# Optimization experiments

Measured on AMD Instinct MI355X. Metric: run time of the kernel, lower is better.

The kernel has to match this reference:

```python
import jax, jax.numpy as jnp
import numpy as np

B, T, D, H = 4, 2048, 1024, 16
HD = D // H  # head_size = 64
EPS = 1e-5


def layernorm(x, g, b):
    mu = jnp.mean(x, axis=-1, keepdims=True)
    var = jnp.var(x, axis=-1, keepdims=True)
    return (x - mu) * jax.lax.rsqrt(var + EPS) * g + b


def setup_inputs() -> dict:
    key = jax.random.key(0)
    ks = jax.random.split(key, 8)
    s = 0.02
    return {
        "x": jax.random.normal(ks[0], (B, T, D), jnp.float32),
        "Wq": jax.random.normal(ks[1], (D, D), jnp.float32) * s,
        "Wk": jax.random.normal(ks[2], (D, D), jnp.float32) * s,
        "Wv": jax.random.normal(ks[3], (D, D), jnp.float32) * s,
        "Wo": jax.random.normal(ks[4], (D, D), jnp.float32) * s,
        "bo": jnp.zeros((D,), jnp.float32),
        "W1": jax.random.normal(ks[5], (D, 4 * D), jnp.float32) * s,
        "b1": jnp.zeros((4 * D,), jnp.float32),
        "W2": jax.random.normal(ks[6], (4 * D, D), jnp.float32) * s,
        "b2": jnp.zeros((D,), jnp.float32),
        "ln1_g": jnp.ones((D,), jnp.float32),
        "ln1_b": jnp.zeros((D,), jnp.float32),
        "ln2_g": jnp.ones((D,), jnp.float32),
        "ln2_b": jnp.zeros((D,), jnp.float32),
    }


def reference(x, Wq, Wk, Wv, Wo, bo, W1, b1, W2, b2, ln1_g, ln1_b, ln2_g, ln2_b):
    # --- multi-head causal self-attention (pre-LN), dropout off (eval) ---
    h = layernorm(x, ln1_g, ln1_b)
    q = jnp.einsum('btd,de->bte', h, Wq).reshape(B, T, H, HD)
    k = jnp.einsum('btd,de->bte', h, Wk).reshape(B, T, H, HD)
    v = jnp.einsum('btd,de->bte', h, Wv).reshape(B, T, H, HD)
    scores = jnp.einsum('bqhd,bkhd->bhqk', q, k) * (HD ** -0.5)
    causal = jnp.tril(jnp.ones((T, T), bool))
    scores = jnp.where(causal, scores, -jnp.inf)
    attn = jax.nn.softmax(scores, axis=-1)
    out = jnp.einsum('bhqk,bkhd->bqhd', attn, v).reshape(B, T, D)
    out = jnp.einsum('btd,de->bte', out, Wo) + bo
    x = x + out
    # --- feed-forward: Linear -> ReLU -> Linear -> ReLU (as in source) ---
    h2 = layernorm(x, ln2_g, ln2_b)
    ff = jax.nn.relu(jnp.einsum('btd,df->btf', h2, W1) + b1)
    ff = jax.nn.relu(jnp.einsum('btf,fd->btd', ff, W2) + b2)
    return x + ff
```

## Files before the change

### kernel.cpp

```cpp
#include <hip/hip_runtime.h>
#include <cstdint>
#include <cstddef>

typedef unsigned short u16;
typedef __attribute__((ext_vector_type(8))) short bf16x8;
typedef __attribute__((ext_vector_type(4))) float f32x4;
typedef __attribute__((address_space(1))) const unsigned int gu32;
typedef __attribute__((address_space(3))) unsigned int lu32;

#define QSCALE 0.1803368801111204f

__device__ __forceinline__ u16 f2bf(float f) {
  uint32_t u = __float_as_uint(f);
  u += 0x7fffu + ((u >> 16) & 1u);
  return (u16)(u >> 16);
}

__global__ __launch_bounds__(256) void transpose_w(const float* __restrict__ W,
                                                   u16* __restrict__ WT,
                                                   int K, int N) {
  __shared__ float t[32][33];
  int n0 = blockIdx.x * 32, k0 = blockIdx.y * 32;
  for (int i = threadIdx.y; i < 32; i += 8)
    t[i][threadIdx.x] = W[(size_t)(k0 + i) * N + n0 + threadIdx.x];
  __syncthreads();
  for (int i = threadIdx.y; i < 32; i += 8)
    WT[(size_t)(n0 + i) * K + k0 + threadIdx.x] = f2bf(t[threadIdx.x][i]);
}

__global__ __launch_bounds__(256) void ln_kernel(const float* __restrict__ x,
                                                 const float* __restrict__ g,
                                                 const float* __restrict__ b,
                                                 u16* __restrict__ out) {
  int row = blockIdx.x;
  const float4 v = *(const float4*)(x + (size_t)row * 1024 + threadIdx.x * 4);
  float s = v.x + v.y + v.z + v.w;
  float ss = v.x * v.x + v.y * v.y + v.z * v.z + v.w * v.w;
#pragma unroll
  for (int d = 1; d < 64; d <<= 1) { s += __shfl_xor(s, d); ss += __shfl_xor(ss, d); }
  __shared__ float rs_[4], rss_[4];
  int wv = threadIdx.x >> 6;
  if ((threadIdx.x & 63) == 0) { rs_[wv] = s; rss_[wv] = ss; }
  __syncthreads();
  s = rs_[0] + rs_[1] + rs_[2] + rs_[3];
  ss = rss_[0] + rss_[1] + rss_[2] + rss_[3];
  float mu = s * (1.f / 1024.f);
  float var = ss * (1.f / 1024.f) - mu * mu;
  float rstd = rsqrtf(var + 1e-5f);
  float4 gv = *(const float4*)(g + threadIdx.x * 4);
  float4 bv = *(const float4*)(b + threadIdx.x * 4);
  uint32_t lo = (uint32_t)f2bf((v.x - mu) * rstd * gv.x + bv.x) |
                ((uint32_t)f2bf((v.y - mu) * rstd * gv.y + bv.y) << 16);
  uint32_t hi = (uint32_t)f2bf((v.z - mu) * rstd * gv.z + bv.z) |
                ((uint32_t)f2bf((v.w - mu) * rstd * gv.w + bv.w) << 16);
  uint2 o; o.x = lo; o.y = hi;
  *(uint2*)(out + (size_t)row * 1024 + threadIdx.x * 4) = o;
}

#define STAGEA(slot, tnext, is)                                               \
  __builtin_amdgcn_global_load_lds(                                           \
      (gu32*)((const char*)(A + (size_t)(bm * 256 + (is) * 64 + srow) * K +   \
                            (size_t)(tnext) * 64) + ssw),                     \
      (lu32*)&lds[(slot) * 24576 + (is) * 4096 + wid * 512], 16, 0, 0)
#define STAGEB(slot, tnext, is)                                               \
  __builtin_amdgcn_global_load_lds(                                           \
      (gu32*)((const char*)(BT + (size_t)(bn * 128 + (is) * 64 + srow) * K +  \
                            (size_t)(tnext) * 64) + ssw),                     \
      (lu32*)&lds[(slot) * 24576 + 16384 + (is) * 4096 + wid * 512], 16, 0, 0)

template <int MODE>
__global__ __launch_bounds__(512, 2) void gemm8p(
    const u16* __restrict__ A, const u16* __restrict__ BT,
    int M, int N, int K,
    const float* __restrict__ bias, const float* __restrict__ resid,
    float* __restrict__ outf,
    u16* __restrict__ ob0, u16* __restrict__ ob1, u16* __restrict__ ob2) {
  __shared__ __align__(16) u16 lds[73728];
  const int tid = threadIdx.x, lane = tid & 63, wid = tid >> 6;
  const int wr = wid >> 1, wc = wid & 1;
  const int bm = blockIdx.y, bn = blockIdx.x;
  const int l15 = lane & 15, lhi = lane >> 4;
  const int srow = tid >> 3;
  const int ssw = ((tid & 7) * 16) ^ ((srow & 7) << 4);
  const int cs0 = (lhi * 8) ^ ((l15 & 7) << 3);
  const int cs1 = (32 + lhi * 8) ^ ((l15 & 7) << 3);
  const int arow = (wr * 64 + l15) * 64;
  const int brow = (wc * 64 + l15) * 64;

  f32x4 acc[4][4];
#pragma unroll
  for (int i = 0; i < 4; ++i)
#pragma unroll
    for (int j = 0; j < 4; ++j) acc[i][j] = (f32x4){0.f, 0.f, 0.f, 0.f};

  const int NT = K >> 6;

#pragma unroll
  for (int t0 = 0; t0 < 2; ++t0) {
    STAGEA(t0, t0, 0); STAGEA(t0, t0, 1); STAGEA(t0, t0, 2); STAGEA(t0, t0, 3);
    STAGEB(t0, t0, 0); STAGEB(t0, t0, 1);
  }
  asm volatile("s_waitcnt vmcnt(6)" ::: "memory");
  __builtin_amdgcn_s_barrier();

  int s = 0, sn = 2;
  for (int t = 0; t < NT; ++t) {
    const bool hasPre = (t + 2) < NT;
    const int aoff = s * 24576, boff = s * 24576 + 16384;

    bf16x8 bfr[4][2], afr[2][2];
#pragma unroll
    for (int ni = 0; ni < 4; ++ni) {
      bfr[ni][0] = *(const bf16x8*)&lds[boff + brow + ni * 1024 + cs0];
      bfr[ni][1] = *(const bf16x8*)&lds[boff + brow + ni * 1024 + cs1];
    }
    afr[0][0] = *(const bf16x8*)&lds[aoff + arow + cs0];
    afr[0][1] = *(const bf16x8*)&lds[aoff + arow + cs1];
    afr[1][0] = *(const bf16x8*)&lds[aoff + arow + 1024 + cs0];
    afr[1][1] = *(const bf16x8*)&lds[aoff + arow + 1024 + cs1];
    if (hasPre) { STAGEA(sn, t + 2, 0); STAGEA(sn, t + 2, 1); STAGEB(sn, t + 2, 0); }
    __builtin_amdgcn_s_barrier();
    __builtin_amdgcn_s_setprio(1);
#pragma unroll
    for (int ks = 0; ks < 2; ++ks)
#pragma unroll
      for (int ml = 0; ml < 2; ++ml)
#pragma unroll
        for (int ni = 0; ni < 4; ++ni)
          acc[ml][ni] = __builtin_amdgcn_mfma_f32_16x16x32_bf16(afr[ml][ks], bfr[ni][ks], acc[ml][ni], 0, 0, 0);
    __builtin_amdgcn_s_setprio(0);
    __builtin_amdgcn_s_barrier();

    afr[0][0] = *(const bf16x8*)&lds[aoff + arow + 2048 + cs0];
    afr[0][1] = *(const bf16x8*)&lds[aoff + arow + 2048 + cs1];
    afr[1][0] = *(const bf16x8*)&lds[aoff + arow + 3072 + cs0];
    afr[1][1] = *(const bf16x8*)&lds[aoff + arow + 3072 + cs1];
    if (hasPre) { STAGEA(sn, t + 2, 2); STAGEA(sn, t + 2, 3); STAGEB(sn, t + 2, 1); }
    __builtin_amdgcn_s_barrier();
    __builtin_amdgcn_s_setprio(1);
#pragma unroll
    for (int ks = 0; ks < 2; ++ks)
#pragma unroll
      for (int ml = 0; ml < 2; ++ml)
#pragma unroll
        for (int ni = 0; ni < 4; ++ni)
          acc[2 + ml][ni] = __builtin_amdgcn_mfma_f32_16x16x32_bf16(afr[ml][ks], bfr[ni][ks], acc[2 + ml][ni], 0, 0, 0);
    __builtin_amdgcn_s_setprio(0);
    if (hasPre) {
      asm volatile("s_waitcnt vmcnt(6)" ::: "memory");
    } else if (t + 1 < NT) {
      asm volatile("s_waitcnt vmcnt(0)" ::: "memory");
    }
    __builtin_amdgcn_s_barrier();

    s = (s == 2) ? 0 : s + 1;
    sn = (sn == 2) ? 0 : sn + 1;
  }

  if (MODE == 0) {
    char* ep = (char*)lds;
    const bool vmode = (bn >= 16);
    if (vmode) {
#pragma unroll
      for (int mi = 0; mi < 4; ++mi)
#pragma unroll
        for (int ni = 0; ni < 4; ++ni) {
          uint32_t lo, hi;
          asm("v_cvt_pk_bf16_f32 %0, %1, %2"
              : "=v"(lo) : "v"(acc[mi][ni][0]), "v"(acc[mi][ni][1]));
          asm("v_cvt_pk_bf16_f32 %0, %1, %2"
              : "=v"(hi) : "v"(acc[mi][ni][2]), "v"(acc[mi][ni][3]));
          uint2 pk; pk.x = lo; pk.y = hi;
          int c_local = wc * 64 + ni * 16 + l15;
          int rb = wr * 64 + mi * 16 + lhi * 4;
          *(uint2*)(ep + c_local * 528 + rb * 2) = pk;
        }
    } else {
      const float sc = (bn < 8) ? QSCALE : 1.f;
#pragma unroll
      for (int mi = 0; mi < 4; ++mi)
#pragma unroll
        for (int ni = 0; ni < 4; ++ni) {
          int c_local = wc * 64 + ni * 16 + l15;
          int rb = wr * 64 + mi * 16 + lhi * 4;
#pragma unroll
          for (int r = 0; r < 4; ++r) {
            *(u16*)(ep + (rb + r) * 272 + c_local * 2) = f2bf(acc[mi][ni][r] * sc);
          }
        }
    }
    __syncthreads();
    if (vmode) {
#pragma unroll
      for (int i = 0; i < 8; ++i) {
        int idx = i * 512 + tid;
        int c = idx >> 5, tc = idx & 31;
        uint4 d4 = *(const uint4*)(ep + c * 528 + tc * 16);
        int cm = bn * 128 + c - 2048, hh = cm >> 6, dd = cm & 63;
        size_t bh = (size_t)((bm >> 3) * 16 + hh);
        int t0 = (bm & 7) * 256;
        *(uint4*)&ob2[(bh * 64 + dd) * 2048 + t0 + tc * 8] = d4;
      }
    } else {
#pragma unroll
      for (int i = 0; i < 8; ++i) {
        int idx = i * 512 + tid;
        int row = idx >> 4, cc = idx & 15;
        uint4 d4 = *(const uint4*)(ep + row * 272 + cc * 16);
        size_t rg = (size_t)(bm * 256 + row);
        int colg = bn * 128 + cc * 8;
        if (colg < 1024)
          *(uint4*)&ob0[rg * 1024 + colg] = d4;
        else
          *(uint4*)&ob1[rg * 1024 + colg - 1024] = d4;
      }
    }
  } else {
#pragma unroll
    for (int mi = 0; mi < 4; ++mi) {
#pragma unroll
      for (int ni = 0; ni < 4; ++ni) {
        int col = bn * 128 + wc * 64 + ni * 16 + l15;
        int rbase = bm * 256 + wr * 64 + mi * 16 + lhi * 4;
#pragma unroll
        for (int r = 0; r < 4; ++r) {
          float v = acc[mi][ni][r];
          int rg = rbase + r;
          if (MODE == 1) {
            outf[(size_t)rg * N + col] = v + bias[col] + resid[(size_t)rg * N + col];
          } else {
            outf[(size_t)rg * N + col] = fmaxf(v + bias[col], 0.f) + resid[(size_t)rg * N + col];
          }
        }
      }
    }
  }
}

#define SA32(slot, t, inst)                                                   \
  __builtin_amdgcn_global_load_lds(                                           \
      (gu32*)((const char*)(A + (size_t)(bm * 256 + (inst) * 128 +            \
                            (tid >> 2)) * K + (size_t)(t) * 32) + ssw2),      \
      (lu32*)&lds[(slot) * 16384 + (inst) * 4096 + tid * 8], 16, 0, 0)
#define SB32(slot, t, inst)                                                   \
  __builtin_amdgcn_global_load_lds(                                           \
      (gu32*)((const char*)(BT + (size_t)(bn * 256 + (inst) * 128 +           \
                            (tid >> 2)) * K + (size_t)(t) * 32) + ssw2),      \
      (lu32*)&lds[(slot) * 16384 + 8192 + (inst) * 4096 + tid * 8], 16, 0, 0)
#define STAGE32(slot, t)                                                      \
  do { SA32(slot, t, 0); SA32(slot, t, 1); SB32(slot, t, 0); SB32(slot, t, 1); } while (0)

__global__ __launch_bounds__(512, 2) void gemm256k32(
    const u16* __restrict__ A, const u16* __restrict__ BT,
    int M, int N, int K,
    const float* __restrict__ bias, u16* __restrict__ out) {
  __shared__ __align__(16) u16 lds[65536];
  const int tid = threadIdx.x, lane = tid & 63, wid = tid >> 6;
  const int wr = wid >> 2, wc = wid & 3;
  const int bm = blockIdx.y, bn = blockIdx.x;
  const int l15 = lane & 15, lhi = lane >> 4;
  const int ssw2 = ((tid & 3) * 16) ^ (((tid >> 2) & 3) << 4);
  const int cb = (lhi * 16) ^ ((l15 & 3) << 4);

  f32x4 acc[8][4];
#pragma unroll
  for (int i = 0; i < 8; ++i)
#pragma unroll
    for (int j = 0; j < 4; ++j) acc[i][j] = (f32x4){0.f, 0.f, 0.f, 0.f};

  const int NT = K >> 5;

  STAGE32(0, 0); STAGE32(1, 1); STAGE32(2, 2);

  for (int t = 0; t < NT; ++t) {
    if (t + 3 < NT) STAGE32((t + 3) & 3, t + 3);
    const int ahead = NT - 1 - t;
    if (ahead >= 3)      asm volatile("s_waitcnt vmcnt(12)" ::: "memory");
    else if (ahead == 2) asm volatile("s_waitcnt vmcnt(8)" ::: "memory");
    else if (ahead == 1) asm volatile("s_waitcnt vmcnt(4)" ::: "memory");
    else                 asm volatile("s_waitcnt vmcnt(0)" ::: "memory");
    __builtin_amdgcn_s_barrier();

    const char* Ap = (const char*)lds + (size_t)(t & 3) * 32768;
    const char* Bp = Ap + 16384;
    bf16x8 bfr[4], afr[8];
#pragma unroll
    for (int nf = 0; nf < 4; ++nf)
      bfr[nf] = *(const bf16x8*)(Bp + (wc * 64 + nf * 16 + l15) * 64 + cb);
#pragma unroll
    for (int mf = 0; mf < 8; ++mf)
      afr[mf] = *(const bf16x8*)(Ap + (wr * 128 + mf * 16 + l15) * 64 + cb);
    __builtin_amdgcn_s_setprio(1);
#pragma unroll
    for (int mf = 0; mf < 8; ++mf)
#pragma unroll
      for (int nf = 0; nf < 4; ++nf)
        acc[mf][nf] = __builtin_amdgcn_mfma_f32_16x16x32_bf16(afr[mf], bfr[nf], acc[mf][nf], 0, 0, 0);
    __builtin_amdgcn_s_setprio(0);
    __builtin_amdgcn_s_barrier();
  }

  char* ep = (char*)lds;
#pragma unroll
  for (int h = 0; h < 2; ++h) {
    __syncthreads();
    if (wr == h) {
#pragma unroll
      for (int ni = 0; ni < 4; ++ni) {
        int c_local = wc * 64 + ni * 16 + l15;
        float bv = bias[bn * 256 + c_local];
#pragma unroll
        for (int mi = 0; mi < 8; ++mi) {
          int rb = mi * 16 + lhi * 4;
#pragma unroll
          for (int r = 0; r < 4; ++r) {
            float v = fmaxf(acc[mi][ni][r] + bv, 0.f);
            *(u16*)(ep + (rb + r) * 528 + c_local * 2) = f2bf(v);
          }
        }
      }
    }
    __syncthreads();
#pragma unroll
    for (int i = 0; i < 8; ++i) {
      int idx = i * 512 + tid;
      int row = idx >> 5, cc = idx & 31;
      uint4 d4 = *(const uint4*)(ep + row * 528 + cc * 16);
      size_t rg = (size_t)(bm * 256 + h * 128 + row);
      *(uint4*)&out[rg * (size_t)N + bn * 256 + cc * 8] = d4;
    }
  }
}

__global__ __launch_bounds__(512) void attn_kernel(
    const u16* __restrict__ Qb, const u16* __restrict__ Kb,
    const u16* __restrict__ VTb, u16* __restrict__ O) {
  const int p = blockIdx.x;
  const int bh = blockIdx.y;
  const int b = bh >> 4, h = bh & 15;
  const u16* Q = Qb + (size_t)b * 2048 * 1024 + h * 64;
  const u16* Kn = Kb + (size_t)b * 2048 * 1024 + h * 64;
  const u16* VT = VTb + (size_t)bh * 64 * 2048;
  const int tid = threadIdx.x, lane = tid & 63, wv = tid >> 6;
  const int l15 = lane & 15, lhi = lane >> 4;
  const int srow = tid >> 3;
  const int scol16 = (tid & 7) * 16;
  const int sw = scol16 ^ ((srow & 7) << 4);
  const int rswz = (l15 & 7) << 4;
  const int cb0 = (lhi * 16) ^ rswz;
  const int cb1 = (64 + lhi * 16) ^ rswz;

  __shared__ __align__(16) u16 KV[2][2][4096];
  __shared__ u16 Ps[8][16 * 72];

#define STAGEKV(slot, kt)                                                     \
  do {                                                                        \
    __builtin_amdgcn_global_load_lds(                                         \
        (gu32*)((const char*)(Kn + (size_t)((kt)*64 + srow) * 1024) + sw),    \
        (lu32*)&KV[slot][0][wv * 512], 16, 0, 0);                             \
    __builtin_amdgcn_global_load_lds(                                         \
        (gu32*)((const char*)(VT + (size_t)srow * 2048 + (kt)*64) + sw),      \
        (lu32*)&KV[slot][1][wv * 512], 16, 0, 0);                             \
  } while (0)

#pragma unroll
  for (int pass = 0; pass < 2; ++pass) {
    const int chunk = pass ? p : (15 - p);
    const int qbase = chunk * 128 + wv * 16;
    const int nkt = 2 * chunk + 2;

    bf16x8 qf[2];
#pragma unroll
    for (int ks = 0; ks < 2; ++ks)
      qf[ks] = *(const bf16x8*)&Q[(size_t)(qbase + l15) * 1024 + ks * 32 + lhi * 8];

    f32x4 o[4];
#pragma unroll
    for (int f = 0; f < 4; ++f) o[f] = (f32x4){0.f, 0.f, 0.f, 0.f};
    float m = -1e30f;
    float l = 0.f;

    __syncthreads();
    STAGEKV(0, 0);

    for (int kt = 0; kt < nkt; ++kt) {
      const int cs = kt & 1;
      asm volatile("s_waitcnt vmcnt(0)" ::: "memory");
      __syncthreads();
      if (kt + 1 < nkt) STAGEKV(cs ^ 1, kt + 1);

      if (kt * 64 <= qbase + 15) {
        const char* Kbase = (const char*)&KV[cs][0][0];
        const char* Vbase = (const char*)&KV[cs][1][0];

        f32x4 s[4];
#pragma unroll
        for (int jt = 0; jt < 4; ++jt) s[jt] = (f32x4){0.f, 0.f, 0.f, 0.f};
        __builtin_amdgcn_s_setprio(1);
#pragma unroll
        for (int ks = 0; ks < 2; ++ks) {
          const int cbyte = ks ? cb1 : cb0;
#pragma unroll
          for (int jt = 0; jt < 4; ++jt) {
            bf16x8 kf = *(const bf16x8*)(Kbase + (jt * 16 + l15) * 128 + cbyte);
            s[jt] = __builtin_amdgcn_mfma_f32_16x16x32_bf16(kf, qf[ks], s[jt], 0, 0, 0);
          }
        }
        __builtin_amdgcn_s_setprio(0);

        if (kt * 64 + 63 > qbase) {
          int qg = qbase + l15;
#pragma unroll
          for (int jt = 0; jt < 4; ++jt)
#pragma unroll
            for (int r = 0; r < 4; ++r) {
              int kg = kt * 64 + jt * 16 + lhi * 4 + r;
              if (kg > qg) s[jt][r] = -1e30f;
            }
        }

        float mr = fmaxf(fmaxf(s[0][0], s[0][1]), fmaxf(s[0][2], s[0][3]));
#pragma unroll
        for (int jt = 1; jt < 4; ++jt)
          mr = fmaxf(mr, fmaxf(fmaxf(s[jt][0], s[jt][1]), fmaxf(s[jt][2], s[jt][3])));
        mr = fmaxf(mr, __shfl_xor(mr, 16));
        mr = fmaxf(mr, __shfl_xor(mr, 32));
        if (__any(mr > m + 8.f)) {
          float mn = fmaxf(m, mr);
          float sc = exp2f(m - mn);
          l *= sc;
          m = mn;
#pragma unroll
          for (int r = 0; r < 4; ++r) {
            float so = __shfl(sc, lhi * 4 + r);
#pragma unroll
            for (int f = 0; f < 4; ++f) o[f][r] *= so;
          }
        }

        float rs = 0.f;
#pragma unroll
        for (int jt = 0; jt < 4; ++jt)
#pragma unroll
          for (int r = 0; r < 4; ++r) {
            float pv = exp2f(s[jt][r] - m);
            s[jt][r] = pv;
            rs += pv;
          }
        rs += __shfl_xor(rs, 16);
        rs += __shfl_xor(rs, 32);
        l += rs;

#pragma unroll
        for (int jt = 0; jt < 4; ++jt) {
          uint32_t lo, hi;
          asm("v_cvt_pk_bf16_f32 %0, %1, %2"
              : "=v"(lo) : "v"(s[jt][0]), "v"(s[jt][1]));
          asm("v_cvt_pk_bf16_f32 %0, %1, %2"
              : "=v"(hi) : "v"(s[jt][2]), "v"(s[jt][3]));
          uint2 pk; pk.x = lo; pk.y = hi;
          *(uint2*)&Ps[wv][l15 * 72 + jt * 16 + lhi * 4] = pk;
        }
        __builtin_amdgcn_s_setprio(1);
#pragma unroll
        for (int ks = 0; ks < 2; ++ks) {
          const int cbyte = ks ? cb1 : cb0;
          bf16x8 pf = *(const bf16x8*)&Ps[wv][l15 * 72 + ks * 32 + lhi * 8];
#pragma unroll
          for (int f = 0; f < 4; ++f) {
            bf16x8 vfr = *(const bf16x8*)(Vbase + (f * 16 + l15) * 128 + cbyte);
            o[f] = __builtin_amdgcn_mfma_f32_16x16x32_bf16(pf, vfr, o[f], 0, 0, 0);
          }
        }
        __builtin_amdgcn_s_setprio(0);
      }
    }

#pragma unroll
    for (int r = 0; r < 4; ++r) {
      float ld = __shfl(l, lhi * 4 + r);
      float inv = 1.f / ld;
      int t = qbase + lhi * 4 + r;
#pragma unroll
      for (int f = 0; f < 4; ++f)
        O[((size_t)(b * 2048 + t)) * 1024 + h * 64 + f * 16 + l15] = f2bf(o[f][r] * inv);
    }
  }
#undef STAGEKV
}

extern "C" void kernel_launch(void* const* d_in, const int* in_sizes, int n_in,
                              void* d_out, int out_size, void* d_ws, size_t ws_size,
                              hipStream_t stream) {
  const float* x   = (const float*)d_in[0];
  const float* Wq  = (const float*)d_in[1];
  const float* Wk  = (const float*)d_in[2];
  const float* Wv  = (const float*)d_in[3];
  const float* Wo  = (const float*)d_in[4];
  const float* bo  = (const float*)d_in[5];
  const float* W1  = (const float*)d_in[6];
  const float* b1  = (const float*)d_in[7];
  const float* W2  = (const float*)d_in[8];
  const float* b2  = (const float*)d_in[9];
  const float* g1  = (const float*)d_in[10];
  const float* be1 = (const float*)d_in[11];
  const float* g2  = (const float*)d_in[12];
  const float* be2 = (const float*)d_in[13];

  char* p = (char*)d_ws;
  auto alloc = [&](size_t bytes) {
    char* r = p;
    p += (bytes + 255) & ~(size_t)255;
    return r;
  };
  u16* WqkvT = (u16*)alloc(3072ull * 1024 * 2);
  u16* WoT   = (u16*)alloc(1024ull * 1024 * 2);
  u16* W1T   = (u16*)alloc(4096ull * 1024 * 2);
  u16* W2T   = (u16*)alloc(1024ull * 4096 * 2);
  u16* hln   = (u16*)alloc(8192ull * 1024 * 2);
  u16* Qbuf  = (u16*)alloc(8192ull * 1024 * 2);
  u16* Kbuf  = (u16*)alloc(8192ull * 1024 * 2);
  u16* VTbuf = (u16*)alloc(8192ull * 1024 * 2);
  float* x2  = (float*)alloc(8192ull * 1024 * 4);
  u16* ff1   = (u16*)alloc(8192ull * 4096 * 2);
  u16* Oattn = hln;
  u16* h2    = Qbuf;
  if ((size_t)(p - (char*)d_ws) > ws_size) return;

  dim3 tb(32, 8);
  transpose_w<<<dim3(32, 32), tb, 0, stream>>>(Wq, WqkvT, 1024, 1024);
  transpose_w<<<dim3(32, 32), tb, 0, stream>>>(Wk, WqkvT + 1024 * 1024, 1024, 1024);
  transpose_w<<<dim3(32, 32), tb, 0, stream>>>(Wv, WqkvT + 2048 * 1024, 1024, 1024);
  transpose_w<<<dim3(32, 32), tb, 0, stream>>>(Wo, WoT, 1024, 1024);
  transpose_w<<<dim3(128, 32), tb, 0, stream>>>(W1, W1T, 1024, 4096);
  transpose_w<<<dim3(32, 128), tb, 0, stream>>>(W2, W2T, 4096, 1024);

  ln_kernel<<<8192, 256, 0, stream>>>(x, g1, be1, hln);

  gemm8p<0><<<dim3(24, 32), 512, 0, stream>>>(hln, WqkvT, 8192, 3072, 1024,
                                              nullptr, nullptr, nullptr,
                                              Qbuf, Kbuf, VTbuf);

  attn_kernel<<<dim3(8, 64), 512, 0, stream>>>(Qbuf, Kbuf, VTbuf, Oattn);

  gemm8p<1><<<dim3(8, 32), 512, 0, stream>>>(Oattn, WoT, 8192, 1024, 1024,
                                             bo, x, x2, nullptr, nullptr, nullptr);

  ln_kernel<<<8192, 256, 0, stream>>>(x2, g2, be2, h2);

  gemm256k32<<<dim3(16, 32), 512, 0, stream>>>(h2, W1T, 8192, 4096, 1024, b1, ff1);

  gemm8p<3><<<dim3(8, 32), 512, 0, stream>>>(ff1, W2T, 8192, 1024, 4096,
                                             b2, x2, (float*)d_out, nullptr, nullptr, nullptr);
}
```

Measured before the change: 400.8 us.

## Software-pipeline LDS fragment loads in FFN1 GEMM and change LDS swizzle

```diff
diff --git a/kernel.cpp b/kernel.cpp
--- a/kernel.cpp
+++ b/kernel.cpp
@@ -250,7 +250,7 @@
 #define STAGE32(slot, t)                                                      \
   do { SA32(slot, t, 0); SA32(slot, t, 1); SB32(slot, t, 0); SB32(slot, t, 1); } while (0)
 
-__global__ __launch_bounds__(512, 2) void gemm256k32(
+__global__ __launch_bounds__(512, 2) void gemm256p(
     const u16* __restrict__ A, const u16* __restrict__ BT,
     int M, int N, int K,
     const float* __restrict__ bias, u16* __restrict__ out) {
@@ -259,8 +259,8 @@
   const int wr = wid >> 2, wc = wid & 3;
   const int bm = blockIdx.y, bn = blockIdx.x;
   const int l15 = lane & 15, lhi = lane >> 4;
-  const int ssw2 = ((tid & 3) * 16) ^ (((tid >> 2) & 3) << 4);
-  const int cb = (lhi * 16) ^ ((l15 & 3) << 4);
+  const int ssw2 = ((tid & 3) * 16) ^ (((tid >> 3) & 3) << 4);
+  const int cb = (lhi * 16) ^ (((l15 >> 1) & 3) << 4);
 
   f32x4 acc[8][4];
 #pragma unroll
@@ -271,34 +271,65 @@
   const int NT = K >> 5;
 
   STAGE32(0, 0); STAGE32(1, 1); STAGE32(2, 2);
-
-  for (int t = 0; t < NT; ++t) {
-    if (t + 3 < NT) STAGE32((t + 3) & 3, t + 3);
-    const int ahead = NT - 1 - t;
-    if (ahead >= 3)      asm volatile("s_waitcnt vmcnt(12)" ::: "memory");
-    else if (ahead == 2) asm volatile("s_waitcnt vmcnt(8)" ::: "memory");
-    else if (ahead == 1) asm volatile("s_waitcnt vmcnt(4)" ::: "memory");
-    else                 asm volatile("s_waitcnt vmcnt(0)" ::: "memory");
-    __builtin_amdgcn_s_barrier();
-
-    const char* Ap = (const char*)lds + (size_t)(t & 3) * 32768;
+  asm volatile("s_waitcnt vmcnt(8)" ::: "memory");
+  __builtin_amdgcn_s_barrier();
+
+  bf16x8 bfr0[4], afr0[4], bfr1[4], afr1[4], afr2[4];
+  {
+    const char* Ap = (const char*)lds;
     const char* Bp = Ap + 16384;
-    bf16x8 bfr[4], afr[8];
 #pragma unroll
     for (int nf = 0; nf < 4; ++nf)
-      bfr[nf] = *(const bf16x8*)(Bp + (wc * 64 + nf * 16 + l15) * 64 + cb);
-#pragma unroll
-    for (int mf = 0; mf < 8; ++mf)
-      afr[mf] = *(const bf16x8*)(Ap + (wr * 128 + mf * 16 + l15) * 64 + cb);
-    __builtin_amdgcn_s_setprio(1);
-#pragma unroll
-    for (int mf = 0; mf < 8; ++mf)
-#pragma unroll
-      for (int nf = 0; nf < 4; ++nf)
-        acc[mf][nf] = __builtin_amdgcn_mfma_f32_16x16x32_bf16(afr[mf], bfr[nf], acc[mf][nf], 0, 0, 0);
-    __builtin_amdgcn_s_setprio(0);
-    __builtin_amdgcn_s_barrier();
-  }
+      bfr0[nf] = *(const bf16x8*)(Bp + (wc * 64 + nf * 16 + l15) * 64 + cb);
+#pragma unroll
+    for (int mf = 0; mf < 4; ++mf)
+      afr0[mf] = *(const bf16x8*)(Ap + (wr * 128 + mf * 16 + l15) * 64 + cb);
+  }
+
+#define BODY32(t, bfrC, afrC, bfrN, afrN)                                      \
+  {                                                                            \
+    const char* Ap = (const char*)lds + (size_t)((t) & 3) * 32768;             \
+    if ((t) + 3 < NT) STAGE32(((t) + 3) & 3, (t) + 3);                         \
+                        \
+    _Pragma("unroll")                                                          \
+    for (int mf = 0; mf < 4; ++mf)                                             \
+      afr2[mf] = *(const bf16x8*)(Ap + (wr * 128 + (4 + mf) * 16 + l15) * 64 + cb); \
+    __builtin_amdgcn_s_setprio(1);                                             \
+    _Pragma("unroll")                                                          \
+    for (int mf = 0; mf < 4; ++mf)                                             \
+      _Pragma("unroll")                                                        \
+      for (int nf = 0; nf < 4; ++nf)                                           \
+        acc[mf][nf] = __builtin_amdgcn_mfma_f32_16x16x32_bf16(afrC[mf], bfrC[nf], acc[mf][nf], 0, 0, 0); \
+    __builtin_amdgcn_s_setprio(0);                                             \
+    if ((t) + 3 < NT)      asm volatile("s_waitcnt vmcnt(8)" ::: "memory");    \
+    else if ((t) + 2 < NT) asm volatile("s_waitcnt vmcnt(4)" ::: "memory");    \
+    else if ((t) + 1 < NT) asm volatile("s_waitcnt vmcnt(0)" ::: "memory");    \
+    __builtin_amdgcn_s_barrier();                                              \
+               \
+    if ((t) + 1 < NT) {                                                        \
+      const char* Apn = (const char*)lds + (size_t)(((t) + 1) & 3) * 32768;    \
+      const char* Bpn = Apn + 16384;                                           \
+      _Pragma("unroll")                                                        \
+      for (int nf = 0; nf < 4; ++nf)                                           \
+        bfrN[nf] = *(const bf16x8*)(Bpn + (wc * 64 + nf * 16 + l15) * 64 + cb); \
+      _Pragma("unroll")                                                        \
+      for (int mf = 0; mf < 4; ++mf)                                           \
+        afrN[mf] = *(const bf16x8*)(Apn + (wr * 128 + mf * 16 + l15) * 64 + cb); \
+    }                                                                          \
+    __builtin_amdgcn_s_setprio(1);                                             \
+    _Pragma("unroll")                                                          \
+    for (int mf = 0; mf < 4; ++mf)                                             \
+      _Pragma("unroll")                                                        \
+      for (int nf = 0; nf < 4; ++nf)                                           \
+        acc[4 + mf][nf] = __builtin_amdgcn_mfma_f32_16x16x32_bf16(afr2[mf], bfrC[nf], acc[4 + mf][nf], 0, 0, 0); \
+    __builtin_amdgcn_s_setprio(0);                                             \
+  }
+
+  for (int tt = 0; tt < NT; tt += 2) {
+    BODY32(tt, bfr0, afr0, bfr1, afr1);
+    BODY32(tt + 1, bfr1, afr1, bfr0, afr0);
+  }
+#undef BODY32
 
   char* ep = (char*)lds;
 #pragma unroll
@@ -548,7 +579,7 @@
 
   ln_kernel<<<8192, 256, 0, stream>>>(x2, g2, be2, h2);
 
-  gemm256k32<<<dim3(16, 32), 512, 0, stream>>>(h2, W1T, 8192, 4096, 1024, b1, ff1);
+  gemm256p<<<dim3(16, 32), 512, 0, stream>>>(h2, W1T, 8192, 4096, 1024, b1, ff1);
 
   gemm8p<3><<<dim3(8, 32), 512, 0, stream>>>(ff1, W2T, 8192, 1024, 4096,
                                              b2, x2, (float*)d_out, nullptr, nullptr, nullptr);
```

Result: no change. 396.1 us (-1.2%).
